# Optimization experiments

Measured on AMD Instinct MI355X. Metric: run time of the kernel, lower is better.

The kernel has to match this reference:

```python
import jax, jax.numpy as jnp
import numpy as np

EPS = 1e-7
BETA = 1.0


def setup_inputs() -> dict:
    key = jax.random.key(0)
    k1, k2, k3, k4 = jax.random.split(key, 4)
    N, E, D_IN, D_OUT = 50000, 800000, 96, 96
    feat = jax.random.normal(k1, (N, D_IN), dtype=jnp.float32)
    src = jax.random.randint(k2, (E,), 0, N, dtype=jnp.int32)
    dst = jax.random.randint(k3, (E,), 0, N, dtype=jnp.int32)
    W = jax.random.normal(k4, (D_IN, D_OUT), dtype=jnp.float32) / np.sqrt(D_IN)
    b = jnp.zeros((D_OUT,), dtype=jnp.float32)
    return {"feat": feat, "src": src, "dst": dst, "W": W, "b": b}


def reference(feat, src, dst, W, b):
    # GENConv with softmax aggregation (canonical DeeperGCN semantics):
    # per edge e=(u,v): m_e = relu(h_u) + eps
    #                   a_e = softmax over edges into v of (beta * m_e)  (per feature dim)
    #                   msg_v = sum_e a_e * m_e
    # out = MLP(h + msg), MLP here = single Linear (mlp_layers=1)
    N = feat.shape[0]
    m = jax.nn.relu(feat[src]) + EPS                     # [E, D]
    logits = BETA * m                                    # [E, D]
    # numerically stable segment softmax over incoming edges of each dst node
    seg_max = jax.ops.segment_max(logits, dst, num_segments=N)   # [N, D]
    ex = jnp.exp(logits - seg_max[dst])                  # [E, D]
    denom = jax.ops.segment_sum(ex, dst, num_segments=N)         # [N, D]
    a = ex / denom[dst]                                  # [E, D]
    msg = jax.ops.segment_sum(a * m, dst, num_segments=N)        # [N, D]
    feats = feat + msg                                   # residual
    return feats @ W + b                                 # [N, D_out]
```

## Files before the change

### kernel.cpp

```cpp
#include <hip/hip_runtime.h>

#define D 96
#define EPSV 1e-7f
#define STRIDE 64
#define NB 16
#define TFUSED 192
#define EPB 2048
#define CAP 5120
#define HLP 100

__device__ __forceinline__ unsigned short f32_to_bf16_rtne(float x) {
    unsigned int u = __float_as_uint(x);
    u += 0x7fffu + ((u >> 16) & 1u);
    return (unsigned short)(u >> 16);
}
__device__ __forceinline__ float bf16_to_f32(unsigned short u) {
    return __uint_as_float(((unsigned int)u) << 16);
}

__global__ __launch_bounds__(256) void part_conv(
    const int* __restrict__ src, const int* __restrict__ dst,
    uint* __restrict__ cursor,
    uint* __restrict__ stage,
    int E, int pblk,
    const float* __restrict__ feat, ushort* __restrict__ fb, int total4)
{
    __shared__ uint   hist[256];
    __shared__ uint   scn[256];
    __shared__ uint   xbase[256];
    __shared__ uint   gbase[256];
    __shared__ uint   sorted[EPB];
    __shared__ ushort sbid[EPB];

    int t = threadIdx.x;

    if ((int)blockIdx.x >= pblk) {
        int i = ((int)blockIdx.x - pblk) * 256 + t;
        if (i < total4) {
            const float4 f = reinterpret_cast<const float4*>(feat)[i];
            ushort4 o;
            o.x = f32_to_bf16_rtne(f.x);
            o.y = f32_to_bf16_rtne(f.y);
            o.z = f32_to_bf16_rtne(f.z);
            o.w = f32_to_bf16_rtne(f.w);
            reinterpret_cast<ushort4*>(fb)[i] = o;
        }
        return;
    }

    int e0 = blockIdx.x * EPB;
    int tot = E - e0; if (tot > EPB) tot = EPB;

    hist[t] = 0;
    __syncthreads();

    uint myb[EPB / 256], myrk[EPB / 256], myrec[EPB / 256];
    #pragma unroll
    for (int r = 0; r < EPB / 256; ++r) {
        int i = r * 256 + t;
        if (i < tot) {
            int d = dst[e0 + i];
            int s = src[e0 + i];
            uint b = (uint)d >> 8;
            myb[r]  = b;
            myrk[r] = atomicAdd(&hist[b], 1u);
            myrec[r] = (uint)(s & 0xFFFF) | ((uint)(d & 0xFF) << 16);
        }
    }
    __syncthreads();

    scn[t] = hist[t];
    __syncthreads();
    #pragma unroll
    for (int off = 1; off < 256; off <<= 1) {
        uint v = (t >= off) ? scn[t - off] : 0u;
        __syncthreads();
        scn[t] += v;
        __syncthreads();
    }
    xbase[t] = scn[t] - hist[t];
    if (hist[t] > 0)
        gbase[t] = (uint)t * CAP + atomicAdd(&cursor[t], hist[t]);
    __syncthreads();

    #pragma unroll
    for (int r = 0; r < EPB / 256; ++r) {
        int i = r * 256 + t;
        if (i < tot) {
            uint j = xbase[myb[r]] + myrk[r];
            sorted[j] = myrec[r];
            sbid[j]   = (ushort)myb[r];
        }
    }
    __syncthreads();

    #pragma unroll
    for (int r = 0; r < EPB / 256; ++r) {
        int j = r * 256 + t;
        if (j < tot) {
            uint b = sbid[j];
            uint gaddr = gbase[b] + ((uint)j - xbase[b]);
            if (gaddr - b * CAP < CAP)
                stage[gaddr] = sorted[j];
        }
    }
}

__global__ __launch_bounds__(256) void csr_build(
    const uint* __restrict__ cursor, const uint* __restrict__ stage,
    int* __restrict__ deg, ushort* __restrict__ csr, int N)
{
    __shared__ int ldeg[256];
    int b = blockIdx.x;
    int t = threadIdx.x;
    ldeg[t] = 0;
    __syncthreads();

    int cnt = (int)cursor[b]; if (cnt > CAP) cnt = CAP;
    const uint* sp = stage + (size_t)b * CAP;
    for (int i = t; i < cnt; i += 256) {
        uint rec = sp[i];
        int s  = rec & 0xFFFF;
        int dl = (rec >> 16) & 0xFF;
        int slot = atomicAdd(&ldeg[dl], 1);
        if (slot < STRIDE)
            csr[(size_t)((b << 8) + dl) * STRIDE + slot] = (ushort)s;
    }
    __syncthreads();
    int n = (b << 8) + t;
    if (n < N) deg[n] = min(ldeg[t], STRIDE);
}

__global__ __launch_bounds__(256) void build_fast(
    const float* __restrict__ feat, ushort* __restrict__ fb, int total4,
    const int* __restrict__ src, const int* __restrict__ dst,
    int* __restrict__ deg, ushort* __restrict__ csr, int E)
{
    int i = blockIdx.x * 256 + threadIdx.x;
    if (i < total4) {
        const float4 f = reinterpret_cast<const float4*>(feat)[i];
        ushort4 o;
        o.x = f32_to_bf16_rtne(f.x);
        o.y = f32_to_bf16_rtne(f.y);
        o.z = f32_to_bf16_rtne(f.z);
        o.w = f32_to_bf16_rtne(f.w);
        reinterpret_cast<ushort4*>(fb)[i] = o;
    } else {
        int e = i - total4;
        if (e < E) {
            int d = dst[e];
            int pos = atomicAdd(&deg[d], 1);
            if (pos < STRIDE) csr[(size_t)d * STRIDE + pos] = (ushort)src[e];
        }
    }
}

__global__ __launch_bounds__(TFUSED, 8) void fused_gather_gemm(
    const float* __restrict__ feat,
    const ushort* __restrict__ fb,
    const int* __restrict__ degp,
    const ushort* __restrict__ csr,
    const float* __restrict__ W,
    const float* __restrict__ bias,
    float* __restrict__ out,
    int N)
{
    __shared__ float  hl[NB][HLP];
    __shared__ ushort csr_l[NB * STRIDE];
    __shared__ int    degl[NB];

    int t = threadIdx.x;
    int nb0 = blockIdx.x * NB;

    {
        int nodes = N - nb0; if (nodes > NB) nodes = NB;
        int avail4 = (nodes * STRIDE) / 8;
        const uint4* gsrc = reinterpret_cast<const uint4*>(csr + (size_t)nb0 * STRIDE);
        uint4* ldst = reinterpret_cast<uint4*>(csr_l);
        if (t < avail4) ldst[t] = gsrc[t];
        if (t >= 128 && t < 128 + NB) {
            int nl = t - 128;
            int n = nb0 + nl;
            degl[nl] = (n < N) ? min(degp[n], STRIDE) : 0;
        }
    }
    __syncthreads();

    for (int task = t; task < NB * 24; task += TFUSED) {
        int nl = task / 24;
        int q  = (task % 24) * 4;
        int n  = nb0 + nl;
        if (n >= N) continue;

        int c = degl[nl];
        const ushort* cl = &csr_l[nl * STRIDE];

        float d0 = 0.f, d1 = 0.f, d2 = 0.f, d3 = 0.f;
        float a0 = 0.f, a1 = 0.f, a2 = 0.f, a3 = 0.f;

        #define PROC(u) { \
            float m0 = fmaxf(bf16_to_f32((u).x), 0.f) + EPSV; \
            float m1 = fmaxf(bf16_to_f32((u).y), 0.f) + EPSV; \
            float m2 = fmaxf(bf16_to_f32((u).z), 0.f) + EPSV; \
            float m3 = fmaxf(bf16_to_f32((u).w), 0.f) + EPSV; \
            float e0 = __expf(m0), e1 = __expf(m1), e2 = __expf(m2), e3 = __expf(m3); \
            d0 += e0; d1 += e1; d2 += e2; d3 += e3; \
            a0 = fmaf(e0, m0, a0); a1 = fmaf(e1, m1, a1); \
            a2 = fmaf(e2, m2, a2); a3 = fmaf(e3, m3, a3); }

        int j = 0;
        for (; j + 8 <= c; j += 8) {
            const ushort4 ia = *reinterpret_cast<const ushort4*>(cl + j);
            const ushort4 ib = *reinterpret_cast<const ushort4*>(cl + j + 4);
            const ushort4 u0 = *reinterpret_cast<const ushort4*>(fb + (size_t)ia.x * D + q);
            const ushort4 u1 = *reinterpret_cast<const ushort4*>(fb + (size_t)ia.y * D + q);
            const ushort4 u2 = *reinterpret_cast<const ushort4*>(fb + (size_t)ia.z * D + q);
            const ushort4 u3 = *reinterpret_cast<const ushort4*>(fb + (size_t)ia.w * D + q);
            const ushort4 u4 = *reinterpret_cast<const ushort4*>(fb + (size_t)ib.x * D + q);
            const ushort4 u5 = *reinterpret_cast<const ushort4*>(fb + (size_t)ib.y * D + q);
            const ushort4 u6 = *reinterpret_cast<const ushort4*>(fb + (size_t)ib.z * D + q);
            const ushort4 u7 = *reinterpret_cast<const ushort4*>(fb + (size_t)ib.w * D + q);
            PROC(u0); PROC(u1); PROC(u2); PROC(u3);
            PROC(u4); PROC(u5); PROC(u6); PROC(u7);
        }
        if (j + 4 <= c) {
            const ushort4 ia = *reinterpret_cast<const ushort4*>(cl + j);
            const ushort4 u0 = *reinterpret_cast<const ushort4*>(fb + (size_t)ia.x * D + q);
            const ushort4 u1 = *reinterpret_cast<const ushort4*>(fb + (size_t)ia.y * D + q);
            const ushort4 u2 = *reinterpret_cast<const ushort4*>(fb + (size_t)ia.z * D + q);
            const ushort4 u3 = *reinterpret_cast<const ushort4*>(fb + (size_t)ia.w * D + q);
            PROC(u0); PROC(u1); PROC(u2); PROC(u3);
            j += 4;
        }
        for (; j < c; ++j) {
            int s = cl[j];
            const ushort4 u = *reinterpret_cast<const ushort4*>(fb + (size_t)s * D + q);
            PROC(u);
        }
        #undef PROC

        const float4 base = *reinterpret_cast<const float4*>(feat + (size_t)n * D + q);
        bool has = c > 0;
        float4 hv;
        hv.x = base.x + (has ? a0 / d0 : 0.f);
        hv.y = base.y + (has ? a1 / d1 : 0.f);
        hv.z = base.z + (has ? a2 / d2 : 0.f);
        hv.w = base.w + (has ? a3 / d3 : 0.f);
        *reinterpret_cast<float4*>(&hl[nl][q]) = hv;
    }
    __syncthreads();

    int q   = (t % 24) * 4;
    int grp = t / 24;
    int r0 = grp * 2, r1 = r0 + 1;
    float4 acc0 = *reinterpret_cast<const float4*>(bias + q);
    float4 acc1 = acc0;

    #pragma unroll 4
    for (int k = 0; k < D; ++k) {
        const float4 w = *reinterpret_cast<const float4*>(W + k * D + q);
        float h0 = hl[r0][k];
        float h1 = hl[r1][k];
        acc0.x = fmaf(h0, w.x, acc0.x); acc0.y = fmaf(h0, w.y, acc0.y);
        acc0.z = fmaf(h0, w.z, acc0.z); acc0.w = fmaf(h0, w.w, acc0.w);
        acc1.x = fmaf(h1, w.x, acc1.x); acc1.y = fmaf(h1, w.y, acc1.y);
        acc1.z = fmaf(h1, w.z, acc1.z); acc1.w = fmaf(h1, w.w, acc1.w);
    }

    int n0 = nb0 + r0;
    if (n0 + 0 < N) *reinterpret_cast<float4*>(out + (size_t)(n0 + 0) * D + q) = acc0;
    if (n0 + 1 < N) *reinterpret_cast<float4*>(out + (size_t)(n0 + 1) * D + q) = acc1;
}

extern "C" void kernel_launch(void* const* d_in, const int* in_sizes, int n_in,
                              void* d_out, int out_size, void* d_ws, size_t ws_size,
                              hipStream_t stream) {
    const float* feat = (const float*)d_in[0];
    const int*   src  = (const int*)d_in[1];
    const int*   dst  = (const int*)d_in[2];
    const float* W    = (const float*)d_in[3];
    const float* bias = (const float*)d_in[4];

    int N = in_sizes[0] / D;
    int E = in_sizes[1];
    int total4 = N * D / 4;
    int nbuck  = (N + 255) >> 8;

    size_t fb_bytes    = (size_t)N * D * sizeof(ushort);
    size_t deg_bytes   = (size_t)N * sizeof(int);
    size_t csr_bytes   = (size_t)N * STRIDE * sizeof(ushort);
    size_t cur_bytes   = 256 * sizeof(uint);
    size_t stage_bytes = (size_t)nbuck * CAP * sizeof(uint);

    size_t part_need  = fb_bytes + deg_bytes + csr_bytes + cur_bytes + stage_bytes;
    size_t fast_need  = fb_bytes + deg_bytes + csr_bytes;

    int gblocks = (N + NB - 1) / NB;

    ushort* fb  = (ushort*)d_ws;
    int*    deg = (int*)((char*)d_ws + fb_bytes);
    ushort* csr = (ushort*)((char*)deg + deg_bytes);

    if (ws_size >= part_need) {
        uint* cursor = (uint*)((char*)csr + csr_bytes);
        uint* stage  = (uint*)((char*)cursor + cur_bytes);

        int pblk = (E + EPB - 1) / EPB;
        int cblk = (total4 + 255) / 256;

        (void)hipMemsetAsync(cursor, 0, cur_bytes, stream);
        part_conv<<<pblk + cblk, 256, 0, stream>>>(
            src, dst, cursor, stage, E, pblk, feat, fb, total4);
        csr_build<<<nbuck, 256, 0, stream>>>(cursor, stage, deg, csr, N);
        fused_gather_gemm<<<gblocks, TFUSED, 0, stream>>>(
            feat, fb, deg, csr, W, bias, (float*)d_out, N);
    } else if (ws_size >= fast_need) {
        (void)hipMemsetAsync(deg, 0, deg_bytes, stream);
        int btotal = total4 + E;
        build_fast<<<(btotal + 255) / 256, 256, 0, stream>>>(
            feat, fb, total4, src, dst, deg, csr, E);
        fused_gather_gemm<<<gblocks, TFUSED, 0, stream>>>(
            feat, fb, deg, csr, W, bias, (float*)d_out, N);
    }
}
```

Measured before the change: 87.23 us.

## Split gather into feature-slice pass with transposed CSR and sliced bf16 features

Feature rows are stored as 12 slices of 8 bf16 values, each slice contiguous across nodes, and the CSR is transposed to slot-major, so a separate gather pass handles one node per thread per slice with coalesced index loads. Each slice's working set (~800KB) stays cache resident, which is meant to improve L2 hit rates for the random source gathers. Messages are written as bf16 to a buffer that reuses the staging area, and a separate GEMM kernel adds the residual and applies the linear layer. The cost is an extra kernel launch, a round trip of the message buffer through memory, and an extra bf16 rounding of messages.

```diff
diff --git a/kernel.cpp b/kernel.cpp
--- a/kernel.cpp
+++ b/kernel.cpp
@@ -3,10 +3,11 @@
 #define D 96
 #define EPSV 1e-7f
 #define STRIDE 64
+#define NPAIR 12
+#define EPB 2048
+#define CAP 5120
 #define NB 16
 #define TFUSED 192
-#define EPB 2048
-#define CAP 5120
 #define HLP 100
 
 __device__ __forceinline__ unsigned short f32_to_bf16_rtne(float x) {
@@ -14,6 +15,11 @@
     u += 0x7fffu + ((u >> 16) & 1u);
     return (unsigned short)(u >> 16);
 }
+__device__ __forceinline__ uint pack2(float a, float b) {
+    return (uint)f32_to_bf16_rtne(a) | ((uint)f32_to_bf16_rtne(b) << 16);
+}
+__device__ __forceinline__ float blo(uint u) { return __uint_as_float(u << 16); }
+__device__ __forceinline__ float bhi(uint u) { return __uint_as_float(u & 0xFFFF0000u); }
 __device__ __forceinline__ float bf16_to_f32(unsigned short u) {
     return __uint_as_float(((unsigned int)u) << 16);
 }
@@ -23,7 +29,8 @@
     uint* __restrict__ cursor,
     uint* __restrict__ stage,
     int E, int pblk,
-    const float* __restrict__ feat, ushort* __restrict__ fb, int total4)
+    const float* __restrict__ feat, ushort* __restrict__ fbP,
+    int N, int cpslice)
 {
     __shared__ uint   hist[256];
     __shared__ uint   scn[256];
@@ -35,15 +42,16 @@
     int t = threadIdx.x;
 
     if ((int)blockIdx.x >= pblk) {
-        int i = ((int)blockIdx.x - pblk) * 256 + t;
-        if (i < total4) {
-            const float4 f = reinterpret_cast<const float4*>(feat)[i];
-            ushort4 o;
-            o.x = f32_to_bf16_rtne(f.x);
-            o.y = f32_to_bf16_rtne(f.y);
-            o.z = f32_to_bf16_rtne(f.z);
-            o.w = f32_to_bf16_rtne(f.w);
-            reinterpret_cast<ushort4*>(fb)[i] = o;
+        int cb = (int)blockIdx.x - pblk;
+        int p  = cb / cpslice;
+        int n  = (cb - p * cpslice) * 256 + t;
+        if (p < NPAIR && n < N) {
+            const float4 fa = *reinterpret_cast<const float4*>(feat + (size_t)n * D + p * 8);
+            const float4 fb4 = *reinterpret_cast<const float4*>(feat + (size_t)n * D + p * 8 + 4);
+            uint4 o;
+            o.x = pack2(fa.x, fa.y);  o.y = pack2(fa.z, fa.w);
+            o.z = pack2(fb4.x, fb4.y); o.w = pack2(fb4.z, fb4.w);
+            *reinterpret_cast<uint4*>(fbP + ((size_t)p * N + n) * 8) = o;
         }
         return;
     }
@@ -106,9 +114,9 @@
     }
 }
 
-__global__ __launch_bounds__(256) void csr_build(
+__global__ __launch_bounds__(256) void csr_buildT(
     const uint* __restrict__ cursor, const uint* __restrict__ stage,
-    int* __restrict__ deg, ushort* __restrict__ csr, int N)
+    int* __restrict__ deg, ushort* __restrict__ csrT, int N)
 {
     __shared__ int ldeg[256];
     int b = blockIdx.x;
@@ -124,11 +132,124 @@
         int dl = (rec >> 16) & 0xFF;
         int slot = atomicAdd(&ldeg[dl], 1);
         if (slot < STRIDE)
-            csr[(size_t)((b << 8) + dl) * STRIDE + slot] = (ushort)s;
+            csrT[(size_t)slot * N + (b << 8) + dl] = (ushort)s;
     }
     __syncthreads();
     int n = (b << 8) + t;
     if (n < N) deg[n] = min(ldeg[t], STRIDE);
+}
+
+__global__ __launch_bounds__(256, 4) void gather_pass(
+    const ushort* __restrict__ fbP,
+    const int* __restrict__ deg,
+    const ushort* __restrict__ csrT,
+    ushort* __restrict__ msgP,
+    int N)
+{
+    int b = blockIdx.x;
+    int p = b % NPAIR;
+    int chunk = b / NPAIR;
+    int t = threadIdx.x;
+    int n = chunk * 256 + t;
+    if (n >= N) return;
+
+    int c = deg[n];
+    const ushort* fs = fbP + (size_t)p * N * 8;
+
+    float d0=0.f,d1=0.f,d2=0.f,d3=0.f,d4=0.f,d5=0.f,d6=0.f,d7=0.f;
+    float a0=0.f,a1=0.f,a2=0.f,a3=0.f,a4=0.f,a5=0.f,a6=0.f,a7=0.f;
+
+    #define PROCP(U) { \
+        float m0=fmaxf(blo((U).x),0.f)+EPSV, m1=fmaxf(bhi((U).x),0.f)+EPSV; \
+        float m2=fmaxf(blo((U).y),0.f)+EPSV, m3=fmaxf(bhi((U).y),0.f)+EPSV; \
+        float m4=fmaxf(blo((U).z),0.f)+EPSV, m5=fmaxf(bhi((U).z),0.f)+EPSV; \
+        float m6=fmaxf(blo((U).w),0.f)+EPSV, m7=fmaxf(bhi((U).w),0.f)+EPSV; \
+        float e0=__expf(m0),e1=__expf(m1),e2=__expf(m2),e3=__expf(m3); \
+        float e4=__expf(m4),e5=__expf(m5),e6=__expf(m6),e7=__expf(m7); \
+        d0+=e0;d1+=e1;d2+=e2;d3+=e3;d4+=e4;d5+=e5;d6+=e6;d7+=e7; \
+        a0=fmaf(e0,m0,a0);a1=fmaf(e1,m1,a1);a2=fmaf(e2,m2,a2);a3=fmaf(e3,m3,a3); \
+        a4=fmaf(e4,m4,a4);a5=fmaf(e5,m5,a5);a6=fmaf(e6,m6,a6);a7=fmaf(e7,m7,a7); }
+
+    int j = 0;
+    for (; j + 4 <= c; j += 4) {
+        int s0 = csrT[(size_t)(j + 0) * N + n];
+        int s1 = csrT[(size_t)(j + 1) * N + n];
+        int s2 = csrT[(size_t)(j + 2) * N + n];
+        int s3 = csrT[(size_t)(j + 3) * N + n];
+        const uint4 u0 = *reinterpret_cast<const uint4*>(fs + (size_t)s0 * 8);
+        const uint4 u1 = *reinterpret_cast<const uint4*>(fs + (size_t)s1 * 8);
+        const uint4 u2 = *reinterpret_cast<const uint4*>(fs + (size_t)s2 * 8);
+        const uint4 u3 = *reinterpret_cast<const uint4*>(fs + (size_t)s3 * 8);
+        PROCP(u0); PROCP(u1); PROCP(u2); PROCP(u3);
+    }
+    for (; j < c; ++j) {
+        int s = csrT[(size_t)j * N + n];
+        const uint4 u = *reinterpret_cast<const uint4*>(fs + (size_t)s * 8);
+        PROCP(u);
+    }
+    #undef PROCP
+
+    bool has = c > 0;
+    uint4 mo;
+    mo.x = pack2(has ? a0 / d0 : 0.f, has ? a1 / d1 : 0.f);
+    mo.y = pack2(has ? a2 / d2 : 0.f, has ? a3 / d3 : 0.f);
+    mo.z = pack2(has ? a4 / d4 : 0.f, has ? a5 / d5 : 0.f);
+    mo.w = pack2(has ? a6 / d6 : 0.f, has ? a7 / d7 : 0.f);
+    *reinterpret_cast<uint4*>(msgP + ((size_t)p * N + n) * 8) = mo;
+}
+
+__global__ __launch_bounds__(TFUSED, 8) void gemm_out(
+    const float* __restrict__ feat,
+    const ushort* __restrict__ msgP,
+    const float* __restrict__ W,
+    const float* __restrict__ bias,
+    float* __restrict__ out,
+    int N)
+{
+    __shared__ float hl[NB][HLP];
+
+    int t = threadIdx.x;
+    int nb0 = blockIdx.x * NB;
+
+    {
+        int qp = t / NB;
+        int nl = t % NB;
+        int n  = nb0 + nl;
+        if (qp < NPAIR && n < N) {
+            const float4 fa = *reinterpret_cast<const float4*>(feat + (size_t)n * D + qp * 8);
+            const float4 fb4 = *reinterpret_cast<const float4*>(feat + (size_t)n * D + qp * 8 + 4);
+            const uint4 mu = *reinterpret_cast<const uint4*>(msgP + ((size_t)qp * N + n) * 8);
+            float4 h0, h1;
+            h0.x = fa.x + blo(mu.x);  h0.y = fa.y + bhi(mu.x);
+            h0.z = fa.z + blo(mu.y);  h0.w = fa.w + bhi(mu.y);
+            h1.x = fb4.x + blo(mu.z); h1.y = fb4.y + bhi(mu.z);
+            h1.z = fb4.z + blo(mu.w); h1.w = fb4.w + bhi(mu.w);
+            *reinterpret_cast<float4*>(&hl[nl][qp * 8])     = h0;
+            *reinterpret_cast<float4*>(&hl[nl][qp * 8 + 4]) = h1;
+        }
+    }
+    __syncthreads();
+
+    int q   = (t % 24) * 4;
+    int grp = t / 24;
+    int r0 = grp * 2, r1 = r0 + 1;
+    float4 acc0 = *reinterpret_cast<const float4*>(bias + q);
+    float4 acc1 = acc0;
+
+    #pragma unroll 4
+    for (int k = 0; k < D; ++k) {
+        const float4 w = *reinterpret_cast<const float4*>(W + k * D + q);
+        float h0 = hl[r0][k];
+        float h1 = hl[r1][k];
+        acc0.x = fmaf(h0, w.x, acc0.x); acc0.y = fmaf(h0, w.y, acc0.y);
+        acc0.z = fmaf(h0, w.z, acc0.z); acc0.w = fmaf(h0, w.w, acc0.w);
+        acc1.x = fmaf(h1, w.x, acc1.x); acc1.y = fmaf(h1, w.y, acc1.y);
+        acc1.z = fmaf(h1, w.z, acc1.z); acc1.w = fmaf(h1, w.w, acc1.w);
+    }
+
+    int n0 = nb0 + r0;
+    if (n0 + 0 < N) *reinterpret_cast<float4*>(out + (size_t)(n0 + 0) * D + q) = acc0;
+    if (n0 + 1 < N) *reinterpret_cast<float4*>(out + (size_t)(n0 + 1) * D + q) = acc1;
 }
 
 __global__ __launch_bounds__(256) void build_fast(
@@ -191,13 +312,10 @@
         int q  = (task % 24) * 4;
         int n  = nb0 + nl;
         if (n >= N) continue;
-
         int c = degl[nl];
         const ushort* cl = &csr_l[nl * STRIDE];
-
         float d0 = 0.f, d1 = 0.f, d2 = 0.f, d3 = 0.f;
         float a0 = 0.f, a1 = 0.f, a2 = 0.f, a3 = 0.f;
-
         #define PROC(u) { \
             float m0 = fmaxf(bf16_to_f32((u).x), 0.f) + EPSV; \
             float m1 = fmaxf(bf16_to_f32((u).y), 0.f) + EPSV; \
@@ -207,30 +325,14 @@
             d0 += e0; d1 += e1; d2 += e2; d3 += e3; \
             a0 = fmaf(e0, m0, a0); a1 = fmaf(e1, m1, a1); \
             a2 = fmaf(e2, m2, a2); a3 = fmaf(e3, m3, a3); }
-
         int j = 0;
-        for (; j + 8 <= c; j += 8) {
-            const ushort4 ia = *reinterpret_cast<const ushort4*>(cl + j);
-            const ushort4 ib = *reinterpret_cast<const ushort4*>(cl + j + 4);
-            const ushort4 u0 = *reinterpret_cast<const ushort4*>(fb + (size_t)ia.x * D + q);
-            const ushort4 u1 = *reinterpret_cast<const ushort4*>(fb + (size_t)ia.y * D + q);
-            const ushort4 u2 = *reinterpret_cast<const ushort4*>(fb + (size_t)ia.z * D + q);
-            const ushort4 u3 = *reinterpret_cast<const ushort4*>(fb + (size_t)ia.w * D + q);
-            const ushort4 u4 = *reinterpret_cast<const ushort4*>(fb + (size_t)ib.x * D + q);
-            const ushort4 u5 = *reinterpret_cast<const ushort4*>(fb + (size_t)ib.y * D + q);
-            const ushort4 u6 = *reinterpret_cast<const ushort4*>(fb + (size_t)ib.z * D + q);
-            const ushort4 u7 = *reinterpret_cast<const ushort4*>(fb + (size_t)ib.w * D + q);
-            PROC(u0); PROC(u1); PROC(u2); PROC(u3);
-            PROC(u4); PROC(u5); PROC(u6); PROC(u7);
-        }
-        if (j + 4 <= c) {
+        for (; j + 4 <= c; j += 4) {
             const ushort4 ia = *reinterpret_cast<const ushort4*>(cl + j);
             const ushort4 u0 = *reinterpret_cast<const ushort4*>(fb + (size_t)ia.x * D + q);
             const ushort4 u1 = *reinterpret_cast<const ushort4*>(fb + (size_t)ia.y * D + q);
             const ushort4 u2 = *reinterpret_cast<const ushort4*>(fb + (size_t)ia.z * D + q);
             const ushort4 u3 = *reinterpret_cast<const ushort4*>(fb + (size_t)ia.w * D + q);
             PROC(u0); PROC(u1); PROC(u2); PROC(u3);
-            j += 4;
         }
         for (; j < c; ++j) {
             int s = cl[j];
@@ -238,7 +340,6 @@
             PROC(u);
         }
         #undef PROC
-
         const float4 base = *reinterpret_cast<const float4*>(feat + (size_t)n * D + q);
         bool has = c > 0;
         float4 hv;
@@ -255,7 +356,6 @@
     int r0 = grp * 2, r1 = r0 + 1;
     float4 acc0 = *reinterpret_cast<const float4*>(bias + q);
     float4 acc1 = acc0;
-
     #pragma unroll 4
     for (int k = 0; k < D; ++k) {
         const float4 w = *reinterpret_cast<const float4*>(W + k * D + q);
@@ -266,7 +366,6 @@
         acc1.x = fmaf(h1, w.x, acc1.x); acc1.y = fmaf(h1, w.y, acc1.y);
         acc1.z = fmaf(h1, w.z, acc1.z); acc1.w = fmaf(h1, w.w, acc1.w);
     }
-
     int n0 = nb0 + r0;
     if (n0 + 0 < N) *reinterpret_cast<float4*>(out + (size_t)(n0 + 0) * D + q) = acc0;
     if (n0 + 1 < N) *reinterpret_cast<float4*>(out + (size_t)(n0 + 1) * D + q) = acc1;
@@ -283,43 +382,48 @@
 
     int N = in_sizes[0] / D;
     int E = in_sizes[1];
-    int total4 = N * D / 4;
-    int nbuck  = (N + 255) >> 8;
-
-    size_t fb_bytes    = (size_t)N * D * sizeof(ushort);
-    size_t deg_bytes   = (size_t)N * sizeof(int);
-    size_t csr_bytes   = (size_t)N * STRIDE * sizeof(ushort);
-    size_t cur_bytes   = 256 * sizeof(uint);
-    size_t stage_bytes = (size_t)nbuck * CAP * sizeof(uint);
-
-    size_t part_need  = fb_bytes + deg_bytes + csr_bytes + cur_bytes + stage_bytes;
-    size_t fast_need  = fb_bytes + deg_bytes + csr_bytes;
-
-    int gblocks = (N + NB - 1) / NB;
-
-    ushort* fb  = (ushort*)d_ws;
-    int*    deg = (int*)((char*)d_ws + fb_bytes);
-    ushort* csr = (ushort*)((char*)deg + deg_bytes);
-
-    if (ws_size >= part_need) {
-        uint* cursor = (uint*)((char*)csr + csr_bytes);
-        uint* stage  = (uint*)((char*)cursor + cur_bytes);
+    int nbuck   = (N + 255) >> 8;
+    int cpslice = (N + 255) / 256;
+
+    size_t fbP_b   = (size_t)N * D * 2;
+    size_t csrT_b  = (size_t)N * STRIDE * 2;
+    size_t deg_b   = (size_t)N * 4;
+    size_t cur_b   = 256 * 4;
+    size_t stage_b = (size_t)nbuck * CAP * 4;
+    size_t msgP_b  = (size_t)N * D * 2;
+    size_t tail_b  = stage_b > msgP_b ? stage_b : msgP_b;
+    size_t needT   = fbP_b + csrT_b + deg_b + cur_b + tail_b;
+    size_t needF   = fbP_b + deg_b + csrT_b;
+
+    if (ws_size >= needT) {
+        ushort* fbP    = (ushort*)d_ws;
+        ushort* csrT   = (ushort*)((char*)d_ws + fbP_b);
+        int*    deg    = (int*)((char*)csrT + csrT_b);
+        uint*   cursor = (uint*)((char*)deg + deg_b);
+        uint*   stage  = (uint*)((char*)cursor + cur_b);
+        ushort* msgP   = (ushort*)stage;
 
         int pblk = (E + EPB - 1) / EPB;
-        int cblk = (total4 + 255) / 256;
-
-        (void)hipMemsetAsync(cursor, 0, cur_bytes, stream);
+        int cblk = NPAIR * cpslice;
+
+        (void)hipMemsetAsync(cursor, 0, cur_b, stream);
         part_conv<<<pblk + cblk, 256, 0, stream>>>(
-            src, dst, cursor, stage, E, pblk, feat, fb, total4);
-        csr_build<<<nbuck, 256, 0, stream>>>(cursor, stage, deg, csr, N);
-        fused_gather_gemm<<<gblocks, TFUSED, 0, stream>>>(
-            feat, fb, deg, csr, W, bias, (float*)d_out, N);
-    } else if (ws_size >= fast_need) {
-        (void)hipMemsetAsync(deg, 0, deg_bytes, stream);
+            src, dst, cursor, stage, E, pblk, feat, fbP, N, cpslice);
+        csr_buildT<<<nbuck, 256, 0, stream>>>(cursor, stage, deg, csrT, N);
+        gather_pass<<<NPAIR * cpslice, 256, 0, stream>>>(fbP, deg, csrT, msgP, N);
+        gemm_out<<<(N + NB - 1) / NB, TFUSED, 0, stream>>>(
+            feat, msgP, W, bias, (float*)d_out, N);
+    } else if (ws_size >= needF) {
+        ushort* fb  = (ushort*)d_ws;
+        int*    deg = (int*)((char*)d_ws + fbP_b);
+        ushort* csr = (ushort*)((char*)deg + deg_b);
+        int total4 = N * D / 4;
+
+        (void)hipMemsetAsync(deg, 0, deg_b, stream);
         int btotal = total4 + E;
         build_fast<<<(btotal + 255) / 256, 256, 0, stream>>>(
             feat, fb, total4, src, dst, deg, csr, E);
-        fused_gather_gemm<<<gblocks, TFUSED, 0, stream>>>(
+        fused_gather_gemm<<<(N + NB - 1) / NB, TFUSED, 0, stream>>>(
             feat, fb, deg, csr, W, bias, (float*)d_out, N);
     }
 }
```

Measured after the change: 126.3 us. 1.45x slower.
